# Optimization experiments

Measured on AMD Instinct MI355X. Metric: run time of the kernel, lower is better.

The kernel has to match this reference:

```python
import jax, jax.numpy as jnp
import numpy as np

D_MODEL = 768
NUM_HEADS = 12
D_HEAD = D_MODEL // NUM_HEADS


def setup_inputs() -> dict:
    key = jax.random.key(0)
    ks = jax.random.split(key, 12)
    B, S = 2, 2048
    s = 1.0 / np.sqrt(D_MODEL)
    inp = {
        "query": jax.random.normal(ks[0], (B, S, D_MODEL), dtype=jnp.float32),
        "key": jax.random.normal(ks[1], (B, S, D_MODEL), dtype=jnp.float32),
        "value": jax.random.normal(ks[2], (B, S, D_MODEL), dtype=jnp.float32),
        "mask": jax.random.randint(ks[3], (B, 1, 1, S), 0, 2, dtype=jnp.int32),
        "Wq": jax.random.normal(ks[4], (D_MODEL, D_MODEL), dtype=jnp.float32) * s,
        "bq": jnp.zeros((D_MODEL,), dtype=jnp.float32),
        "Wk": jax.random.normal(ks[5], (D_MODEL, D_MODEL), dtype=jnp.float32) * s,
        "bk": jnp.zeros((D_MODEL,), dtype=jnp.float32),
        "Wv": jax.random.normal(ks[6], (D_MODEL, D_MODEL), dtype=jnp.float32) * s,
        "bv": jnp.zeros((D_MODEL,), dtype=jnp.float32),
        "Wo": jax.random.normal(ks[7], (D_MODEL, D_MODEL), dtype=jnp.float32) * s,
        "bo": jnp.zeros((D_MODEL,), dtype=jnp.float32),
    }
    return inp


def _split_heads(x):
    # [B, S, D] -> [B, H, S, Dh]
    B, S, _ = x.shape
    return x.reshape(B, S, NUM_HEADS, D_HEAD).transpose(0, 2, 1, 3)


def reference(query, key, value, mask, Wq, bq, Wk, bk, Wv, bv, Wo, bo):
    q = _split_heads(query @ Wq + bq)
    k = _split_heads(key @ Wk + bk)
    v = _split_heads(value @ Wv + bv)
    scores = jnp.einsum("bhqd,bhkd->bhqk", q, k) / jnp.sqrt(jnp.float32(D_HEAD))
    scores = jnp.where(mask == 0, -jnp.inf, scores)
    attn = jax.nn.softmax(scores, axis=-1)  # dropout is identity at inference
    ctx = jnp.einsum("bhqk,bhkd->bhqd", attn, v)
    B, _, S, _ = ctx.shape
    ctx = ctx.transpose(0, 2, 1, 3).reshape(B, S, D_MODEL)
    return ctx @ Wo + bo
```

## Files before the change

### kernel.cpp

```cpp
#include <hip/hip_runtime.h>
#include <stdint.h>

#define D_MODEL 768
#define SEQ     2048
#define BATCH   2
#define NHEAD   12
#define DHEAD   64
#define MROWS   (BATCH * SEQ)

typedef __bf16 bf16x8 __attribute__((ext_vector_type(8)));
typedef float  f32x4  __attribute__((ext_vector_type(4)));
typedef unsigned short u16;
typedef u16 u16x4 __attribute__((ext_vector_type(4)));
typedef uint32_t u32;

__device__ __forceinline__ u16 f32_to_bf16(float x) {
    u32 u = __float_as_uint(x);
    u32 r = (u + 0x7FFFu + ((u >> 16) & 1u)) >> 16;
    return (u16)r;
}
__device__ __forceinline__ float bf16_to_f32(u16 h) {
    return __uint_as_float(((u32)h) << 16);
}
__device__ __forceinline__ void split2(float x, u16 &hi, u16 &lo) {
    hi = f32_to_bf16(x);
    lo = f32_to_bf16(x - bf16_to_f32(hi));
}
__device__ __forceinline__ u32 pack2t(float a, float b) {
    return __builtin_amdgcn_perm(__float_as_uint(b), __float_as_uint(a), 0x07060302u);
}

__device__ __forceinline__ void stage16(const u16* g, const u16* l) {
    __builtin_amdgcn_global_load_lds(
        (const __attribute__((address_space(1))) u32*)g,
        (__attribute__((address_space(3))) u32*)l,
        16, 0, 0);
}

#define SRC_C8(lane)  ((((lane) & 3) ^ (((lane) >> 3) & 3)) * 8)
#define RD_C8(quad, l16) (((quad) ^ (((l16) >> 1) & 3)) * 8)

#define QSCALE 0.1803368801111204f
#define MSHIFT 20.0f

__global__ void prep_all(const float* __restrict__ q, const float* __restrict__ k,
                         const float* __restrict__ v, u16* __restrict__ xbase,
                         const float* __restrict__ Wq, const float* __restrict__ Wk,
                         const float* __restrict__ Wv, const float* __restrict__ Wo,
                         u16* __restrict__ wtbase,
                         const int* __restrict__ Mask, float* __restrict__ BiasM)
{
    __shared__ float tile[32][33];
    const int bx = blockIdx.x;
    if (bx < 9216) {
        const int t = bx / 3072;
        const float* src = (t == 0) ? q : (t == 1) ? k : v;
        const size_t P = (size_t)MROWS * D_MODEL;
        u16* xh = xbase + (size_t)t * 2 * P;
        u16* xl = xh + P;
        size_t idx = ((size_t)(bx % 3072) * 256 + threadIdx.x) * 4;
        float4 val = *reinterpret_cast<const float4*>(&src[idx]);
        float vv[4] = {val.x, val.y, val.z, val.w};
        u16x4 h4, l4;
        #pragma unroll
        for (int j = 0; j < 4; ++j) { u16 h, l; split2(vv[j], h, l); h4[j] = h; l4[j] = l; }
        *reinterpret_cast<u16x4*>(&xh[idx]) = h4;
        *reinterpret_cast<u16x4*>(&xl[idx]) = l4;
    } else if (bx < 11520) {
        int r = bx - 9216;
        int w = r / 576; r %= 576;
        int ky = r / 24, nx = r % 24;
        const float* W = (w == 0) ? Wq : (w == 1) ? Wk : (w == 2) ? Wv : Wo;
        const size_t WP = (size_t)D_MODEL * D_MODEL;
        u16* th = wtbase + (size_t)w * 2 * WP;
        u16* tl = th + WP;
        const int tx = threadIdx.x & 31, ty = threadIdx.x >> 5;
        const int n0 = nx * 32, k0 = ky * 32;
        #pragma unroll
        for (int rr = 0; rr < 4; ++rr) {
            int kk = k0 + ty + rr * 8;
            tile[ty + rr * 8][tx] = W[(size_t)kk * D_MODEL + n0 + tx];
        }
        __syncthreads();
        #pragma unroll
        for (int rr = 0; rr < 4; ++rr) {
            int n = n0 + ty + rr * 8;
            float val = tile[tx][ty + rr * 8];
            u16 h, l; split2(val, h, l);
            th[(size_t)n * D_MODEL + k0 + tx] = h;
            tl[(size_t)n * D_MODEL + k0 + tx] = l;
        }
    } else {
        int i = (bx - 11520) * 256 + threadIdx.x;
        BiasM[i] = (Mask[i] == 0) ? -3e38f : -MSHIFT;
    }
}

__global__ __launch_bounds__(256, 4) void gemm3(
    const u16* __restrict__ Ah0, const u16* __restrict__ Al0,
    const u16* __restrict__ Ah1, const u16* __restrict__ Al1,
    const u16* __restrict__ Ah2, const u16* __restrict__ Al2,
    const u16* __restrict__ Bh0, const u16* __restrict__ Bl0,
    const u16* __restrict__ Bh1, const u16* __restrict__ Bl1,
    const u16* __restrict__ Bh2, const u16* __restrict__ Bl2,
    const float* __restrict__ bias0, const float* __restrict__ bias1,
    const float* __restrict__ bias2,
    u16* __restrict__ Qhl, u16* __restrict__ Khl, u16* __restrict__ Vt,
    float* __restrict__ Out, int mode)
{
    const int z = (mode == 3) ? 3 : (int)blockIdx.z;
    const u16 *GAh, *GAl, *GBh, *GBl; const float* Bias;
    if (z == 1)      { GAh = Ah1; GAl = Al1; GBh = Bh1; GBl = Bl1; Bias = bias1; }
    else if (z == 2) { GAh = Ah2; GAl = Al2; GBh = Bh2; GBl = Bl2; Bias = bias2; }
    else             { GAh = Ah0; GAl = Al0; GBh = Bh0; GBl = Bl0; Bias = bias0; }

    const int m0 = blockIdx.x * 128;
    const int n0 = blockIdx.y * 64;
    const int tid  = threadIdx.x;
    const int wave = tid >> 6, lane = tid & 63;
    const int quad = lane >> 4, l16 = lane & 15;
    const int wm = wave & 1, wn = wave >> 1;

    __shared__ u16 sAh[128 * 32];
    __shared__ u16 sAl[128 * 32];
    __shared__ u16 sBh[64 * 32];
    __shared__ u16 sBl[64 * 32];

    const int srow = lane >> 2;
    const int sc8  = SRC_C8(lane);
    const int rc8  = RD_C8(quad, l16);

    f32x4 acc[4][2] = {};

    for (int k0 = 0; k0 < D_MODEL; k0 += 32) {
        {
            #pragma unroll
            for (int i = 0; i < 2; ++i) {
                int row = wave * 32 + i * 16 + srow;
                size_t ga = (size_t)(m0 + row) * D_MODEL + k0 + sc8;
                int ldst = (wave * 32 + i * 16) * 32;
                stage16(&GAh[ga], &sAh[ldst]);
                stage16(&GAl[ga], &sAl[ldst]);
            }
            int row = wave * 16 + srow;
            size_t gb = (size_t)(n0 + row) * D_MODEL + k0 + sc8;
            int ldst = (wave * 16) * 32;
            stage16(&GBh[gb], &sBh[ldst]);
            stage16(&GBl[gb], &sBl[ldst]);
        }
        asm volatile("s_waitcnt vmcnt(0)" ::: "memory");
        __syncthreads();

        bf16x8 afh[4], afl[4], bfh[2], bfl[2];
        #pragma unroll
        for (int t = 0; t < 4; ++t) {
            int ar = wm * 64 + t * 16 + l16;
            afh[t] = *reinterpret_cast<const bf16x8*>(&sAh[ar * 32 + rc8]);
            afl[t] = *reinterpret_cast<const bf16x8*>(&sAl[ar * 32 + rc8]);
        }
        #pragma unroll
        for (int t = 0; t < 2; ++t) {
            int bc = wn * 32 + t * 16 + l16;
            bfh[t] = *reinterpret_cast<const bf16x8*>(&sBh[bc * 32 + rc8]);
            bfl[t] = *reinterpret_cast<const bf16x8*>(&sBl[bc * 32 + rc8]);
        }
        #pragma unroll
        for (int mt = 0; mt < 4; ++mt) {
            #pragma unroll
            for (int nt = 0; nt < 2; ++nt) {
                f32x4 a = acc[mt][nt];
                a = __builtin_amdgcn_mfma_f32_16x16x32_bf16(afh[mt], bfh[nt], a, 0, 0, 0);
                a = __builtin_amdgcn_mfma_f32_16x16x32_bf16(afh[mt], bfl[nt], a, 0, 0, 0);
                a = __builtin_amdgcn_mfma_f32_16x16x32_bf16(afl[mt], bfh[nt], a, 0, 0, 0);
                acc[mt][nt] = a;
            }
        }
        __syncthreads();
    }

    #pragma unroll
    for (int nt = 0; nt < 2; ++nt) {
        int n = n0 + wn * 32 + nt * 16 + l16;
        float bv = Bias[n];
        #pragma unroll
        for (int mt = 0; mt < 4; ++mt) {
            #pragma unroll
            for (int r = 0; r < 4; ++r) {
                int m = m0 + wm * 64 + mt * 16 + quad * 4 + r;
                float v = acc[mt][nt][r] + bv;
                if (mode == 3) {
                    Out[(size_t)m * D_MODEL + n] = v;
                } else {
                    int b = m >> 11, s = m & (SEQ - 1);
                    int h = n >> 6, d = n & 63;
                    size_t bh = (size_t)(b * NHEAD + h);
                    if (z == 0) {
                        u16 hi, lo; split2(v * QSCALE, hi, lo);
                        u16* base = &Qhl[(bh * SEQ + s) * 128];
                        base[d] = hi; base[d + 64] = lo;
                    } else if (z == 1) {
                        u16 hi, lo; split2(v, hi, lo);
                        u16* base = &Khl[(bh * SEQ + s) * 128];
                        base[d] = hi; base[d + 64] = lo;
                    } else {
                        Vt[(bh * DHEAD + d) * SEQ + s] = f32_to_bf16(v);
                    }
                }
            }
        }
    }
}

__global__ __launch_bounds__(256, 3) void attn_kernel(
    const u16* __restrict__ Qhl, const u16* __restrict__ Khl, const u16* __restrict__ Vt,
    const float* __restrict__ BiasM, float* __restrict__ Opart,
    float* __restrict__ Lpart)
{
    const int flat = blockIdx.x;
    const int wk   = (flat & 7) * 96 + (flat >> 3);
    const int qt   = wk & 15;
    const int grp  = wk >> 4;
    const int bh   = grp % 24;
    const int half = grp / 24;
    const int b    = bh / NHEAD;
    const int tid  = threadIdx.x;
    const int wave = tid >> 6, lane = tid & 63;
    const int quad = lane >> 4, l16 = lane & 15;

    __shared__ u16 sK[2][4 * 2048];
    __shared__ u16 sV[2][2 * 2048];

    bf16x8 qh0[2], qh1[2], ql0[2], ql1[2];
    #pragma unroll
    for (int g = 0; g < 2; ++g) {
        const u16* qbase = &Qhl[((size_t)bh * SEQ + qt * 128 + wave * 32 + g * 16 + l16) * 128];
        qh0[g] = *reinterpret_cast<const bf16x8*>(&qbase[quad * 8]);
        qh1[g] = *reinterpret_cast<const bf16x8*>(&qbase[32 + quad * 8]);
        ql0[g] = *reinterpret_cast<const bf16x8*>(&qbase[64 + quad * 8]);
        ql1[g] = *reinterpret_cast<const bf16x8*>(&qbase[96 + quad * 8]);
    }

    union OU { u16 u[8]; bf16x8 v; } onesu;
    #pragma unroll
    for (int j = 0; j < 8; ++j) onesu.u[j] = 0x3F80;
    const bf16x8 ones = onesu.v;

    f32x4 oacc[2][4] = {};
    f32x4 lacc[2] = {};

    const float* biasb = &BiasM[b * SEQ];
    const int srcl0 = (((quad * 2) & 3) << 4) | l16;
    const int srcl1 = (((quad * 2 + 1) & 3) << 4) | l16;
    const bool selhi = (quad >> 1) != 0;

    const int strow = wave * 16 + (lane >> 2);
    const int stc8  = SRC_C8(lane);
    const int rc8   = RD_C8(quad, l16);
    const u16* kgb = &Khl[(size_t)bh * SEQ * 128];
    const u16* vgb = &Vt[(size_t)bh * DHEAD * SEQ];

    const int kvbeg = half * (SEQ / 2);

    #pragma unroll
    for (int j = 0; j < 4; ++j)
        stage16(&kgb[(size_t)(kvbeg + strow) * 128 + j * 32 + stc8],
                &sK[0][j * 2048 + wave * 512]);
    #pragma unroll
    for (int j = 0; j < 2; ++j)
        stage16(&vgb[(size_t)strow * SEQ + kvbeg + j * 32 + stc8],
                &sV[0][j * 2048 + wave * 512]);

    for (int it = 0; it < 16; ++it) {
        const int kv0 = kvbeg + it * 64;
        asm volatile("s_waitcnt vmcnt(0)" ::: "memory");
        __syncthreads();

        if (it + 1 < 16) {
            const int kvn = kv0 + 64;
            u16* dK = sK[(it + 1) & 1];
            u16* dV = sV[(it + 1) & 1];
            #pragma unroll
            for (int j = 0; j < 4; ++j)
                stage16(&kgb[(size_t)(kvn + strow) * 128 + j * 32 + stc8],
                        &dK[j * 2048 + wave * 512]);
            #pragma unroll
            for (int j = 0; j < 2; ++j)
                stage16(&vgb[(size_t)strow * SEQ + kvn + j * 32 + stc8],
                        &dV[j * 2048 + wave * 512]);
        }
        const u16* cK = sK[it & 1];
        const u16* cV = sV[it & 1];

        f32x4 binit[4];
        #pragma unroll
        for (int mt = 0; mt < 4; ++mt) {
            float4 b4 = *reinterpret_cast<const float4*>(
                &biasb[kv0 + mt * 16 + quad * 4]);
            binit[mt][0] = b4.x; binit[mt][1] = b4.y;
            binit[mt][2] = b4.z; binit[mt][3] = b4.w;
        }

        f32x4 sacc[2][4];
        #pragma unroll
        for (int mt = 0; mt < 4; ++mt) {
            const int rb = (mt * 16 + l16) * 32 + rc8;
            bf16x8 kh0 = *reinterpret_cast<const bf16x8*>(&cK[rb]);
            bf16x8 kh1 = *reinterpret_cast<const bf16x8*>(&cK[2048 + rb]);
            bf16x8 kl0 = *reinterpret_cast<const bf16x8*>(&cK[4096 + rb]);
            bf16x8 kl1 = *reinterpret_cast<const bf16x8*>(&cK[6144 + rb]);
            #pragma unroll
            for (int g = 0; g < 2; ++g) {
                f32x4 s = binit[mt];
                s = __builtin_amdgcn_mfma_f32_16x16x32_bf16(kh0, qh0[g], s, 0, 0, 0);
                s = __builtin_amdgcn_mfma_f32_16x16x32_bf16(kh1, qh1[g], s, 0, 0, 0);
                s = __builtin_amdgcn_mfma_f32_16x16x32_bf16(kh0, ql0[g], s, 0, 0, 0);
                s = __builtin_amdgcn_mfma_f32_16x16x32_bf16(kh1, ql1[g], s, 0, 0, 0);
                s = __builtin_amdgcn_mfma_f32_16x16x32_bf16(kl0, qh0[g], s, 0, 0, 0);
                s = __builtin_amdgcn_mfma_f32_16x16x32_bf16(kl1, qh1[g], s, 0, 0, 0);
                sacc[g][mt] = s;
            }
        }

        union FU { u32 u[4]; bf16x8 v; } fr[2][2];
        #pragma unroll
        for (int g = 0; g < 2; ++g) {
            u32 pLo[4], pHi[4];
            #pragma unroll
            for (int mt = 0; mt < 4; ++mt) {
                float p0 = exp2f(sacc[g][mt][0]);
                float p1 = exp2f(sacc[g][mt][1]);
                float p2 = exp2f(sacc[g][mt][2]);
                float p3 = exp2f(sacc[g][mt][3]);
                pLo[mt] = pack2t(p0, p1);
                pHi[mt] = pack2t(p2, p3);
            }
            #pragma unroll
            for (int f = 0; f < 2; ++f) {
                u32 a, bb;
                a  = (u32)__shfl((int)pLo[2 * f],     srcl0, 64);
                bb = (u32)__shfl((int)pLo[2 * f + 1], srcl0, 64);
                fr[g][f].u[0] = selhi ? bb : a;
                a  = (u32)__shfl((int)pHi[2 * f],     srcl0, 64);
                bb = (u32)__shfl((int)pHi[2 * f + 1], srcl0, 64);
                fr[g][f].u[1] = selhi ? bb : a;
                a  = (u32)__shfl((int)pLo[2 * f],     srcl1, 64);
                bb = (u32)__shfl((int)pLo[2 * f + 1], srcl1, 64);
                fr[g][f].u[2] = selhi ? bb : a;
                a  = (u32)__shfl((int)pHi[2 * f],     srcl1, 64);
                bb = (u32)__shfl((int)pHi[2 * f + 1], srcl1, 64);
                fr[g][f].u[3] = selhi ? bb : a;
            }
        }

        #pragma unroll
        for (int dt = 0; dt < 4; ++dt) {
            const int rb = (dt * 16 + l16) * 32 + rc8;
            bf16x8 vb0 = *reinterpret_cast<const bf16x8*>(&cV[rb]);
            bf16x8 vb1 = *reinterpret_cast<const bf16x8*>(&cV[2048 + rb]);
            #pragma unroll
            for (int g = 0; g < 2; ++g) {
                oacc[g][dt] = __builtin_amdgcn_mfma_f32_16x16x32_bf16(vb0, fr[g][0].v, oacc[g][dt], 0, 0, 0);
                oacc[g][dt] = __builtin_amdgcn_mfma_f32_16x16x32_bf16(vb1, fr[g][1].v, oacc[g][dt], 0, 0, 0);
            }
        }
        #pragma unroll
        for (int g = 0; g < 2; ++g) {
            lacc[g] = __builtin_amdgcn_mfma_f32_16x16x32_bf16(ones, fr[g][0].v, lacc[g], 0, 0, 0);
            lacc[g] = __builtin_amdgcn_mfma_f32_16x16x32_bf16(ones, fr[g][1].v, lacc[g], 0, 0, 0);
        }
    }

    #pragma unroll
    for (int g = 0; g < 2; ++g) {
        size_t rowb = ((size_t)(half * (BATCH * NHEAD) + bh)) * SEQ
                    + qt * 128 + wave * 32 + g * 16 + l16;
        float* ob = &Opart[rowb * 64];
        #pragma unroll
        for (int dt = 0; dt < 4; ++dt)
            *reinterpret_cast<f32x4*>(&ob[dt * 16 + quad * 4]) = oacc[g][dt];
        if (quad == 0) Lpart[rowb] = lacc[g][0];
    }
}

__global__ void attn_combine(const float* __restrict__ Opart,
                             const float* __restrict__ Lpart,
                             u16* __restrict__ CTXh, u16* __restrict__ CTXl)
{
    const int NROW = BATCH * NHEAD * SEQ;
    int t = blockIdx.x * 256 + threadIdx.x;
    int row = t >> 4;
    int d0 = (t & 15) << 2;
    float inv = 1.f / (Lpart[row] + Lpart[NROW + row]);
    f32x4 O0 = *reinterpret_cast<const f32x4*>(&Opart[(size_t)row * 64 + d0]);
    f32x4 O1 = *reinterpret_cast<const f32x4*>(&Opart[((size_t)NROW + row) * 64 + d0]);
    int bh = row >> 11, q = row & (SEQ - 1);
    int b = bh / NHEAD, h = bh % NHEAD;
    size_t off = ((size_t)(b * SEQ + q)) * D_MODEL + h * DHEAD + d0;
    u16x4 h4, l4;
    #pragma unroll
    for (int j = 0; j < 4; ++j) {
        float val = (O0[j] + O1[j]) * inv;
        u16 hi, lo; split2(val, hi, lo);
        h4[j] = hi; l4[j] = lo;
    }
    *reinterpret_cast<u16x4*>(&CTXh[off]) = h4;
    *reinterpret_cast<u16x4*>(&CTXl[off]) = l4;
}

extern "C" void kernel_launch(void* const* d_in, const int* in_sizes, int n_in,
                              void* d_out, int out_size, void* d_ws, size_t ws_size,
                              hipStream_t stream)
{
    const float* query = (const float*)d_in[0];
    const float* key   = (const float*)d_in[1];
    const float* value = (const float*)d_in[2];
    const int*   mask  = (const int*)d_in[3];
    const float* Wq = (const float*)d_in[4];
    const float* bq = (const float*)d_in[5];
    const float* Wk = (const float*)d_in[6];
    const float* bk = (const float*)d_in[7];
    const float* Wv = (const float*)d_in[8];
    const float* bv = (const float*)d_in[9];
    const float* Wo = (const float*)d_in[10];
    const float* bo = (const float*)d_in[11];

    char* ws = (char*)d_ws;
    const size_t P2  = (size_t)MROWS * D_MODEL * 2;
    const size_t WP2 = (size_t)D_MODEL * D_MODEL * 2;

    u16* Xbase = (u16*)ws;
    u16* Xh_q = Xbase;                       u16* Xl_q = (u16*)((char*)Xh_q + P2);
    u16* Xh_k = (u16*)((char*)Xbase + 2*P2); u16* Xl_k = (u16*)((char*)Xh_k + P2);
    u16* Xh_v = (u16*)((char*)Xbase + 4*P2); u16* Xl_v = (u16*)((char*)Xh_v + P2);

    char* wtb = ws + 6 * P2;
    u16* Wh_q = (u16*)wtb;                   u16* Wl_q = (u16*)(wtb + WP2);
    u16* Wh_k = (u16*)(wtb + 2*WP2);         u16* Wl_k = (u16*)(wtb + 3*WP2);
    u16* Wh_v = (u16*)(wtb + 4*WP2);         u16* Wl_v = (u16*)(wtb + 5*WP2);
    u16* Wh_o = (u16*)(wtb + 6*WP2);         u16* Wl_o = (u16*)(wtb + 7*WP2);

    char* qb = wtb + 8 * WP2;
    const size_t QK_BYTES = (size_t)BATCH * NHEAD * SEQ * 128 * 2;
    u16* QhlBuf = (u16*)qb;
    u16* KhlBuf = (u16*)(qb + QK_BYTES);
    u16* VtBuf  = (u16*)(qb + 2 * QK_BYTES);

    char* tail = qb + 2 * QK_BYTES + QK_BYTES / 2;
    float* BiasM = (float*)tail;
    float* Lpart = (float*)(tail + 16384);

    float* Opart = (float*)Xh_k;
    u16* CTXh = Xh_q; u16* CTXl = Xl_q;

    float* out = (float*)d_out;
    dim3 blk(256, 1, 1);

    prep_all<<<dim3(11536), blk, 0, stream>>>(
        query, key, value, Xbase, Wq, Wk, Wv, Wo, (u16*)wtb, mask, BiasM);

    gemm3<<<dim3(32, 12, 3), blk, 0, stream>>>(
        Xh_q, Xl_q, Xh_k, Xl_k, Xh_v, Xl_v,
        Wh_q, Wl_q, Wh_k, Wl_k, Wh_v, Wl_v,
        bq, bk, bv, QhlBuf, KhlBuf, VtBuf, nullptr, 0);

    attn_kernel<<<dim3(768), blk, 0, stream>>>(
        QhlBuf, KhlBuf, VtBuf, BiasM, Opart, Lpart);

    attn_combine<<<dim3(3072), blk, 0, stream>>>(Opart, Lpart, CTXh, CTXl);

    gemm3<<<dim3(32, 12, 1), blk, 0, stream>>>(
        CTXh, CTXl, nullptr, nullptr, nullptr, nullptr,
        Wh_o, Wl_o, nullptr, nullptr, nullptr, nullptr,
        bo, nullptr, nullptr, nullptr, nullptr, nullptr, out, 3);
}
```

Measured before the change: 266.1 us.

## Switch attention kernel to 32x32x16 MFMA tiles with permlane32 swap

Restructures the attention inner loop to use 32x32x16 bf16 MFMA instructions instead of 16x16x32. Each wave now handles 32 query rows as one tile, and the P-fragment relayout uses v_permlane32_swap in place of many __shfl calls. It also adds s_setprio around the MFMA blocks. The goal is fewer MFMA issues, less LDS read traffic per FLOP and far fewer cross-lane shuffles. The cost is 16-wide accumulators that raise register pressure at 3 blocks per SM, and the LDS read indexing now depends on the XOR swizzle matching the staging layout.

```diff
diff --git a/kernel.cpp b/kernel.cpp
--- a/kernel.cpp
+++ b/kernel.cpp
@@ -10,6 +10,7 @@
 
 typedef __bf16 bf16x8 __attribute__((ext_vector_type(8)));
 typedef float  f32x4  __attribute__((ext_vector_type(4)));
+typedef float  f32x16 __attribute__((ext_vector_type(16)));
 typedef unsigned short u16;
 typedef u16 u16x4 __attribute__((ext_vector_type(4)));
 typedef uint32_t u32;
@@ -225,19 +226,19 @@
     const int b    = bh / NHEAD;
     const int tid  = threadIdx.x;
     const int wave = tid >> 6, lane = tid & 63;
-    const int quad = lane >> 4, l16 = lane & 15;
+    const int l32  = lane & 31;
+    const int hi5  = lane >> 5;
+    const int xorv = (l32 >> 1) & 3;
 
     __shared__ u16 sK[2][4 * 2048];
     __shared__ u16 sV[2][2 * 2048];
 
-    bf16x8 qh0[2], qh1[2], ql0[2], ql1[2];
-    #pragma unroll
-    for (int g = 0; g < 2; ++g) {
-        const u16* qbase = &Qhl[((size_t)bh * SEQ + qt * 128 + wave * 32 + g * 16 + l16) * 128];
-        qh0[g] = *reinterpret_cast<const bf16x8*>(&qbase[quad * 8]);
-        qh1[g] = *reinterpret_cast<const bf16x8*>(&qbase[32 + quad * 8]);
-        ql0[g] = *reinterpret_cast<const bf16x8*>(&qbase[64 + quad * 8]);
-        ql1[g] = *reinterpret_cast<const bf16x8*>(&qbase[96 + quad * 8]);
+    const u16* qbase = &Qhl[((size_t)bh * SEQ + qt * 128 + wave * 32 + l32) * 128];
+    bf16x8 qh[4], ql[4];
+    #pragma unroll
+    for (int ds = 0; ds < 4; ++ds) {
+        qh[ds] = *reinterpret_cast<const bf16x8*>(&qbase[ds * 16 + hi5 * 8]);
+        ql[ds] = *reinterpret_cast<const bf16x8*>(&qbase[64 + ds * 16 + hi5 * 8]);
     }
 
     union OU { u16 u[8]; bf16x8 v; } onesu;
@@ -245,17 +246,12 @@
     for (int j = 0; j < 8; ++j) onesu.u[j] = 0x3F80;
     const bf16x8 ones = onesu.v;
 
-    f32x4 oacc[2][4] = {};
-    f32x4 lacc[2] = {};
+    f32x16 oacc[2] = {};
+    f32x16 lacc = {};
 
     const float* biasb = &BiasM[b * SEQ];
-    const int srcl0 = (((quad * 2) & 3) << 4) | l16;
-    const int srcl1 = (((quad * 2 + 1) & 3) << 4) | l16;
-    const bool selhi = (quad >> 1) != 0;
-
     const int strow = wave * 16 + (lane >> 2);
     const int stc8  = SRC_C8(lane);
-    const int rc8   = RD_C8(quad, l16);
     const u16* kgb = &Khl[(size_t)bh * SEQ * 128];
     const u16* vgb = &Vt[(size_t)bh * DHEAD * SEQ];
 
@@ -291,94 +287,84 @@
         const u16* cK = sK[it & 1];
         const u16* cV = sV[it & 1];
 
-        f32x4 binit[4];
-        #pragma unroll
-        for (int mt = 0; mt < 4; ++mt) {
-            float4 b4 = *reinterpret_cast<const float4*>(
-                &biasb[kv0 + mt * 16 + quad * 4]);
-            binit[mt][0] = b4.x; binit[mt][1] = b4.y;
-            binit[mt][2] = b4.z; binit[mt][3] = b4.w;
-        }
-
-        f32x4 sacc[2][4];
-        #pragma unroll
-        for (int mt = 0; mt < 4; ++mt) {
-            const int rb = (mt * 16 + l16) * 32 + rc8;
-            bf16x8 kh0 = *reinterpret_cast<const bf16x8*>(&cK[rb]);
-            bf16x8 kh1 = *reinterpret_cast<const bf16x8*>(&cK[2048 + rb]);
-            bf16x8 kl0 = *reinterpret_cast<const bf16x8*>(&cK[4096 + rb]);
-            bf16x8 kl1 = *reinterpret_cast<const bf16x8*>(&cK[6144 + rb]);
-            #pragma unroll
-            for (int g = 0; g < 2; ++g) {
-                f32x4 s = binit[mt];
-                s = __builtin_amdgcn_mfma_f32_16x16x32_bf16(kh0, qh0[g], s, 0, 0, 0);
-                s = __builtin_amdgcn_mfma_f32_16x16x32_bf16(kh1, qh1[g], s, 0, 0, 0);
-                s = __builtin_amdgcn_mfma_f32_16x16x32_bf16(kh0, ql0[g], s, 0, 0, 0);
-                s = __builtin_amdgcn_mfma_f32_16x16x32_bf16(kh1, ql1[g], s, 0, 0, 0);
-                s = __builtin_amdgcn_mfma_f32_16x16x32_bf16(kl0, qh0[g], s, 0, 0, 0);
-                s = __builtin_amdgcn_mfma_f32_16x16x32_bf16(kl1, qh1[g], s, 0, 0, 0);
-                sacc[g][mt] = s;
-            }
-        }
-
-        union FU { u32 u[4]; bf16x8 v; } fr[2][2];
-        #pragma unroll
-        for (int g = 0; g < 2; ++g) {
-            u32 pLo[4], pHi[4];
-            #pragma unroll
-            for (int mt = 0; mt < 4; ++mt) {
-                float p0 = exp2f(sacc[g][mt][0]);
-                float p1 = exp2f(sacc[g][mt][1]);
-                float p2 = exp2f(sacc[g][mt][2]);
-                float p3 = exp2f(sacc[g][mt][3]);
-                pLo[mt] = pack2t(p0, p1);
-                pHi[mt] = pack2t(p2, p3);
-            }
-            #pragma unroll
-            for (int f = 0; f < 2; ++f) {
-                u32 a, bb;
-                a  = (u32)__shfl((int)pLo[2 * f],     srcl0, 64);
-                bb = (u32)__shfl((int)pLo[2 * f + 1], srcl0, 64);
-                fr[g][f].u[0] = selhi ? bb : a;
-                a  = (u32)__shfl((int)pHi[2 * f],     srcl0, 64);
-                bb = (u32)__shfl((int)pHi[2 * f + 1], srcl0, 64);
-                fr[g][f].u[1] = selhi ? bb : a;
-                a  = (u32)__shfl((int)pLo[2 * f],     srcl1, 64);
-                bb = (u32)__shfl((int)pLo[2 * f + 1], srcl1, 64);
-                fr[g][f].u[2] = selhi ? bb : a;
-                a  = (u32)__shfl((int)pHi[2 * f],     srcl1, 64);
-                bb = (u32)__shfl((int)pHi[2 * f + 1], srcl1, 64);
-                fr[g][f].u[3] = selhi ? bb : a;
-            }
-        }
-
-        #pragma unroll
-        for (int dt = 0; dt < 4; ++dt) {
-            const int rb = (dt * 16 + l16) * 32 + rc8;
-            bf16x8 vb0 = *reinterpret_cast<const bf16x8*>(&cV[rb]);
-            bf16x8 vb1 = *reinterpret_cast<const bf16x8*>(&cV[2048 + rb]);
-            #pragma unroll
-            for (int g = 0; g < 2; ++g) {
-                oacc[g][dt] = __builtin_amdgcn_mfma_f32_16x16x32_bf16(vb0, fr[g][0].v, oacc[g][dt], 0, 0, 0);
-                oacc[g][dt] = __builtin_amdgcn_mfma_f32_16x16x32_bf16(vb1, fr[g][1].v, oacc[g][dt], 0, 0, 0);
-            }
-        }
-        #pragma unroll
-        for (int g = 0; g < 2; ++g) {
-            lacc[g] = __builtin_amdgcn_mfma_f32_16x16x32_bf16(ones, fr[g][0].v, lacc[g], 0, 0, 0);
-            lacc[g] = __builtin_amdgcn_mfma_f32_16x16x32_bf16(ones, fr[g][1].v, lacc[g], 0, 0, 0);
-        }
-    }
-
-    #pragma unroll
-    for (int g = 0; g < 2; ++g) {
+        u32 pk[2][8];
+        #pragma unroll
+        for (int t = 0; t < 2; ++t) {
+            f32x16 s;
+            #pragma unroll
+            for (int g = 0; g < 4; ++g) {
+                float4 b4 = *reinterpret_cast<const float4*>(
+                    &biasb[kv0 + t * 32 + 8 * g + 4 * hi5]);
+                s[4 * g + 0] = b4.x; s[4 * g + 1] = b4.y;
+                s[4 * g + 2] = b4.z; s[4 * g + 3] = b4.w;
+            }
+            const int rowb = (t * 32 + l32) * 32;
+            __builtin_amdgcn_s_setprio(1);
+            #pragma unroll
+            for (int ds = 0; ds < 4; ++ds) {
+                const int c8  = ((((ds & 1) * 2 + hi5) ^ xorv) * 8);
+                const int off = (ds >> 1) * 2048 + rowb + c8;
+                bf16x8 kh = *reinterpret_cast<const bf16x8*>(&cK[off]);
+                bf16x8 kl = *reinterpret_cast<const bf16x8*>(&cK[4096 + off]);
+                s = __builtin_amdgcn_mfma_f32_32x32x16_bf16(kh, qh[ds], s, 0, 0, 0);
+                s = __builtin_amdgcn_mfma_f32_32x32x16_bf16(kh, ql[ds], s, 0, 0, 0);
+                s = __builtin_amdgcn_mfma_f32_32x32x16_bf16(kl, qh[ds], s, 0, 0, 0);
+            }
+            __builtin_amdgcn_s_setprio(0);
+            #pragma unroll
+            for (int m = 0; m < 8; ++m)
+                pk[t][m] = pack2t(exp2f(s[2 * m]), exp2f(s[2 * m + 1]));
+        }
+
+        union FU { u32 u[4]; bf16x8 v; } fr[4];
+        #pragma unroll
+        for (int t = 0; t < 2; ++t) {
+            u32 a0 = pk[t][0], b0 = pk[t][2];
+            u32 a1 = pk[t][1], b1 = pk[t][3];
+            u32 a2 = pk[t][4], b2 = pk[t][6];
+            u32 a3 = pk[t][5], b3 = pk[t][7];
+            asm volatile("v_permlane32_swap_b32 %0, %1" : "+v"(a0), "+v"(b0));
+            asm volatile("v_permlane32_swap_b32 %0, %1" : "+v"(a1), "+v"(b1));
+            asm volatile("v_permlane32_swap_b32 %0, %1" : "+v"(a2), "+v"(b2));
+            asm volatile("v_permlane32_swap_b32 %0, %1" : "+v"(a3), "+v"(b3));
+            fr[2 * t].u[0] = a0; fr[2 * t].u[1] = a1;
+            fr[2 * t].u[2] = b0; fr[2 * t].u[3] = b1;
+            fr[2 * t + 1].u[0] = a2; fr[2 * t + 1].u[1] = a3;
+            fr[2 * t + 1].u[2] = b2; fr[2 * t + 1].u[3] = b3;
+        }
+
+        __builtin_amdgcn_s_setprio(1);
+        #pragma unroll
+        for (int dt = 0; dt < 2; ++dt) {
+            const int drow = (dt * 32 + l32) * 32;
+            #pragma unroll
+            for (int sl = 0; sl < 4; ++sl) {
+                const int c8  = ((((sl & 1) * 2 + hi5) ^ xorv) * 8);
+                const int off = (sl >> 1) * 2048 + drow + c8;
+                bf16x8 vb = *reinterpret_cast<const bf16x8*>(&cV[off]);
+                oacc[dt] = __builtin_amdgcn_mfma_f32_32x32x16_bf16(vb, fr[sl].v, oacc[dt], 0, 0, 0);
+            }
+        }
+        #pragma unroll
+        for (int sl = 0; sl < 4; ++sl)
+            lacc = __builtin_amdgcn_mfma_f32_32x32x16_bf16(ones, fr[sl].v, lacc, 0, 0, 0);
+        __builtin_amdgcn_s_setprio(0);
+    }
+
+    {
         size_t rowb = ((size_t)(half * (BATCH * NHEAD) + bh)) * SEQ
-                    + qt * 128 + wave * 32 + g * 16 + l16;
+                    + qt * 128 + wave * 32 + l32;
         float* ob = &Opart[rowb * 64];
         #pragma unroll
-        for (int dt = 0; dt < 4; ++dt)
-            *reinterpret_cast<f32x4*>(&ob[dt * 16 + quad * 4]) = oacc[g][dt];
-        if (quad == 0) Lpart[rowb] = lacc[g][0];
+        for (int dt = 0; dt < 2; ++dt) {
+            #pragma unroll
+            for (int g = 0; g < 4; ++g) {
+                f32x4 o4 = { oacc[dt][4 * g + 0], oacc[dt][4 * g + 1],
+                             oacc[dt][4 * g + 2], oacc[dt][4 * g + 3] };
+                *reinterpret_cast<f32x4*>(&ob[dt * 32 + 8 * g + 4 * hi5]) = o4;
+            }
+        }
+        if (lane < 32) Lpart[rowb] = lacc[0];
     }
 }
 
```

Result: no change. 263.0 us (-1.2%).
